# Performance work log

Hardware: AMD Instinct MI355X
Metric: run time of the kernel (lower is better)

## Reference

```python
import jax, jax.numpy as jnp
import numpy as np

N, IN_DIM, H1, H2, HEADS = 3072, 256, 128, 64, 4
NEG_INF = -9.0e15  # matches torch zero_vec = -9e15

def _xavier(key, shape):
    fan_in, fan_out = shape[-2], shape[-1]
    lim = np.sqrt(6.0 / (fan_in + fan_out)).astype(np.float32)
    return jax.random.uniform(key, shape, jnp.float32, -lim, lim)

def setup_inputs() -> dict:
    key = jax.random.key(0)
    ks = jax.random.split(key, 14)
    x = jax.random.normal(ks[0], (N, IN_DIM), jnp.float32)
    adj = jax.random.randint(ks[1], (N, N), 0, 2, jnp.int32)
    # layer 1 params (per-head stacked)
    W1 = _xavier(ks[2], (HEADS, IN_DIM, H1))
    a1s = _xavier(ks[3], (HEADS, H1)) * 1.414   # a[:F] of the (2F,1) xavier vector
    a1d = _xavier(ks[4], (HEADS, H1)) * 1.414   # a[F:]
    lin1 = _xavier(ks[5], (HEADS * H1, H1))
    res1 = _xavier(ks[6], (IN_DIM, H1))
    # layer 2 params
    W2 = _xavier(ks[7], (HEADS, H1, H2))
    a2s = _xavier(ks[8], (HEADS, H2)) * 1.414
    a2d = _xavier(ks[9], (HEADS, H2)) * 1.414
    lin2 = _xavier(ks[10], (HEADS * H2, H2))
    res2 = _xavier(ks[11], (H1, H2))
    return {"x": x, "adj": adj, "W1": W1, "a1s": a1s, "a1d": a1d,
            "lin1": lin1, "res1": res1, "W2": W2, "a2s": a2s, "a2d": a2d,
            "lin2": lin2, "res2": res2}

def _gat_residual_layer(h, mask, W, a_s, a_d, lin, res):
    # h: [N, F_in], W: [H, F_in, F_out], mask: [N, N] bool
    Wh = jnp.einsum('nf,hfo->hno', h, W)                 # [H, N, F_out]
    src = jnp.einsum('hno,ho->hn', Wh, a_s)              # Wh @ a[:F]
    dst = jnp.einsum('hno,ho->hn', Wh, a_d)              # Wh @ a[F:]
    e = src[:, :, None] + dst[:, None, :]                # [H, N, N]
    e = jnp.where(e > 0, e, 0.2 * e)                     # leaky_relu(0.2)
    e = jnp.where(mask[None], e, NEG_INF)                # adj mask
    attn = jax.nn.softmax(e, axis=-1)                    # dropout p=0.1 -> identity (eval)
    hp = jax.nn.elu(jnp.einsum('hij,hjo->hio', attn, Wh))  # per-head output, elu
    n = h.shape[0]
    hp = jnp.transpose(hp, (1, 0, 2)).reshape(n, -1)     # concat heads (head-major)
    hp = jax.nn.elu(hp @ lin)                            # multi-head mix + elu
    out = jax.nn.relu(hp + h @ res)                      # residual + relu
    return jax.nn.relu(out)                              # encoder-loop relu; dropout(0.4) identity

def reference(x, adj, W1, a1s, a1d, lin1, res1, W2, a2s, a2d, lin2, res2):
    mask = adj > 0
    h = _gat_residual_layer(x, mask, W1, a1s, a1d, lin1, res1)
    h = _gat_residual_layer(h, mask, W2, a2s, a2d, lin2, res2)
    return h  # embedding [N, H2]
```

## Files before the change

### kernel.cpp

```cpp
#include <hip/hip_runtime.h>
#include <hip/hip_bf16.h>
#include <stdint.h>

using bf16 = __hip_bfloat16;
typedef short short8 __attribute__((ext_vector_type(8)));
typedef short short4v __attribute__((ext_vector_type(4)));
typedef float f32x4 __attribute__((ext_vector_type(4)));

constexpr int N = 3072;
constexpr int D0 = 256;
constexpr int F1 = 128;
constexpr int F2 = 64;
constexpr int HEADS = 4;
constexpr int NW = N / 32;
constexpr float CSHIFT = 20.0f;

#define DI __device__ __forceinline__
DI short f2bs(float v) { bf16 b = __float2bfloat16(v); return *(short*)&b; }

__global__ __launch_bounds__(256) void k_pack_adj(const int* __restrict__ adj,
                                                  uint32_t* __restrict__ bits) {
  int idx = blockIdx.x * 256 + threadIdx.x;
  unsigned long long m = __ballot(adj[idx] > 0);
  if ((threadIdx.x & 63) == 0) {
    bits[idx >> 5]       = (uint32_t)m;
    bits[(idx >> 5) + 1] = (uint32_t)(m >> 32);
  }
}

__global__ __launch_bounds__(256) void k_cvt(const float* __restrict__ x,
                                             const float* __restrict__ W1,
                                             const float* __restrict__ lin1,
                                             const float* __restrict__ res1,
                                             const float* __restrict__ W2,
                                             const float* __restrict__ lin2,
                                             const float* __restrict__ res2,
                                             bf16* __restrict__ xb,
                                             bf16* __restrict__ W1T,
                                             bf16* __restrict__ lin1T,
                                             bf16* __restrict__ res1T,
                                             bf16* __restrict__ W2T,
                                             bf16* __restrict__ lin2T,
                                             bf16* __restrict__ res2T) {
  int t = blockIdx.y;
  int i = blockIdx.x * 256 + threadIdx.x;
  switch (t) {
    case 0:
      if (i < N * D0) xb[i] = __float2bfloat16(x[i]);
      break;
    case 1:
      if (i < HEADS * F1 * D0) { int k = i & 255; int ho = i >> 8; int h = ho >> 7, o = ho & 127;
        W1T[i] = __float2bfloat16(W1[((size_t)h * D0 + k) * F1 + o]); }
      break;
    case 2:
      if (i < F1 * HEADS * F1) { int k = i & 511; int o = i >> 9;
        lin1T[i] = __float2bfloat16(lin1[k * F1 + o]); }
      break;
    case 3:
      if (i < F1 * D0) { int k = i & 255; int o = i >> 8;
        res1T[i] = __float2bfloat16(res1[k * F1 + o]); }
      break;
    case 4:
      if (i < HEADS * F2 * F1) { int k = i & 127; int ho = i >> 7; int h = ho >> 6, o = ho & 63;
        W2T[i] = __float2bfloat16(W2[((size_t)h * F1 + k) * F2 + o]); }
      break;
    case 5:
      if (i < F2 * HEADS * F2) { int k = i & 255; int o = i >> 8;
        lin2T[i] = __float2bfloat16(lin2[k * F2 + o]); }
      break;
    case 6:
      if (i < F2 * F1) { int k = i & 127; int o = i >> 7;
        res2T[i] = __float2bfloat16(res2[k * F2 + o]); }
      break;
  }
}

template <int K, int NOUT, int F>
__global__ __launch_bounds__(256) void k_whead_mfma(const bf16* __restrict__ A,
                                                    const bf16* __restrict__ BT,
                                                    bf16* __restrict__ BP,
                                                    const float* __restrict__ as_,
                                                    const float* __restrict__ ad_,
                                                    float* __restrict__ src,
                                                    float* __restrict__ dst) {
  int row0 = blockIdx.x * 16;
  int wid = threadIdx.x >> 6, lane = threadIdx.x & 63;
  int l15 = lane & 15, q = lane >> 4;
  int col = blockIdx.y * 64 + wid * 16 + l15;

  const bf16* aP = A + (size_t)(row0 + l15) * K + q * 8;
  const bf16* bP = BT + (size_t)col * K + q * 8;
  f32x4 acc;
#pragma unroll
  for (int r = 0; r < 4; r++) acc[r] = 0.f;
#pragma unroll
  for (int ks = 0; ks < K / 32; ks++) {
    short8 a = *(const short8*)(aP + ks * 32);
    short8 b = *(const short8*)(bP + ks * 32);
    acc = __builtin_amdgcn_mfma_f32_16x16x32_bf16(a, b, acc, 0, 0, 0);
  }

  int h  = col / F;
  int cl = col % F;
  int ct = cl >> 4;
  int jt = row0 >> 5;
  int qp = ((row0 >> 4) & 1) * 2 + (q >> 1);
  int eo = (q & 1) * 4;
  short4v w;
#pragma unroll
  for (int r = 0; r < 4; r++) w[r] = f2bs(acc[r]);
  size_t off = ((((size_t)h * (F / 16) + ct) * (N / 32) + jt) * 4 + qp) * 128 + l15 * 8 + eo;
  *(short4v*)(BP + off) = w;

  float asv = as_[col], adv = ad_[col];
#pragma unroll
  for (int r = 0; r < 4; r++) {
    float sp = acc[r] * asv, dp = acc[r] * adv;
#pragma unroll
    for (int m = 1; m < 16; m <<= 1) {
      sp += __shfl_xor(sp, m);
      dp += __shfl_xor(dp, m);
    }
    if (l15 == 0) {
      atomicAdd(&src[h * N + row0 + q * 4 + r], sp);
      atomicAdd(&dst[h * N + row0 + q * 4 + r], dp);
    }
  }
}

template <int F>
__global__ __launch_bounds__(256, 2) void k_attn_fused(const bf16* __restrict__ BP,
                                                       const float* __restrict__ src,
                                                       const float* __restrict__ dst,
                                                       const uint32_t* __restrict__ bits,
                                                       float* __restrict__ hp_part,
                                                       float* __restrict__ rs_part) {
  constexpr int CT = F / 16;
  constexpr int CTN = CT / 4;
  constexpr int KSTEPS = 12;
  int h    = blockIdx.y;
  int kb   = blockIdx.z;
  int row0 = blockIdx.x * 32;
  int tid = threadIdx.x, wid = tid >> 6, lane = tid & 63;
  int l15 = lane & 15, q = lane >> 4;
  int jbase = kb * (N / 2) + wid * 384;

  float src0 = src[h * N + row0 + l15];
  float src1 = src[h * N + row0 + 16 + l15];
  const float* dh = dst + h * N;
  const uint32_t* b0 = bits + (size_t)(row0 + l15) * NW;
  const uint32_t* b1 = bits + (size_t)(row0 + 16 + l15) * NW;
  const bf16* bph = BP + (size_t)h * CT * (N / 32) * 512;

  f32x4 acc0[CT], acc1[CT];
#pragma unroll
  for (int ct = 0; ct < CT; ct++)
#pragma unroll
    for (int r = 0; r < 4; r++) { acc0[ct][r] = 0.f; acc1[ct][r] = 0.f; }
  float rs0 = 0.f, rs1 = 0.f;

  for (int ks = 0; ks < KSTEPS; ks++) {
    int j0 = jbase + ks * 32;
    int jt = j0 >> 5;
    f32x4 dlo = *(const f32x4*)(dh + j0 + q * 8);
    f32x4 dhi = *(const f32x4*)(dh + j0 + q * 8 + 4);
    uint32_t m0 = (b0[jt] >> (q * 8)) & 0xffu;
    uint32_t m1 = (b1[jt] >> (q * 8)) & 0xffu;
    float pv0[8], pv1[8];
#pragma unroll
    for (int e = 0; e < 8; e++) {
      float d = e < 4 ? dlo[e] : dhi[e - 4];
      float t0 = src0 + d; t0 = fmaxf(t0, 0.2f * t0);
      float p0 = ((m0 >> e) & 1u) ? __expf(t0 - CSHIFT) : 0.f;
      rs0 += p0; pv0[e] = p0;
      float t1 = src1 + d; t1 = fmaxf(t1, 0.2f * t1);
      float p1 = ((m1 >> e) & 1u) ? __expf(t1 - CSHIFT) : 0.f;
      rs1 += p1; pv1[e] = p1;
    }
    short8 a0, a1;
#pragma unroll
    for (int e = 0; e < 8; e++) { a0[e] = f2bs(pv0[e]); a1[e] = f2bs(pv1[e]); }
#pragma unroll
    for (int ct = 0; ct < CT; ct++) {
      short8 b = *(const short8*)(bph + (((size_t)ct * (N / 32) + jt) * 64 + lane) * 8);
      acc0[ct] = __builtin_amdgcn_mfma_f32_16x16x32_bf16(a0, b, acc0[ct], 0, 0, 0);
      acc1[ct] = __builtin_amdgcn_mfma_f32_16x16x32_bf16(a1, b, acc1[ct], 0, 0, 0);
    }
  }

  rs0 += __shfl_xor(rs0, 16); rs0 += __shfl_xor(rs0, 32);
  rs1 += __shfl_xor(rs1, 16); rs1 += __shfl_xor(rs1, 32);
  if (q == 0) atomicAdd(&rs_part[((size_t)kb * HEADS + h) * N + row0 + l15], rs0);
  if (q == 1) atomicAdd(&rs_part[((size_t)kb * HEADS + h) * N + row0 + 16 + l15], rs1);

  __shared__ float red[4][64][CT * 4 + 1];
#pragma unroll
  for (int t = 0; t < 2; t++) {
    __syncthreads();
#pragma unroll
    for (int ct = 0; ct < CT; ct++)
#pragma unroll
      for (int r = 0; r < 4; r++)
        red[wid][lane][ct * 4 + r] = t ? acc1[ct][r] : acc0[ct][r];
    __syncthreads();
#pragma unroll
    for (int cc = 0; cc < CTN; cc++) {
      int ct = wid * CTN + cc;
#pragma unroll
      for (int r = 0; r < 4; r++) {
        float v = red[0][lane][ct * 4 + r] + red[1][lane][ct * 4 + r] +
                  red[2][lane][ct * 4 + r] + red[3][lane][ct * 4 + r];
        int row = row0 + t * 16 + q * 4 + r;
        hp_part[((size_t)kb * N + row) * (HEADS * F) + h * F + ct * 16 + l15] = v;
      }
    }
  }
}

template <int F>
__global__ __launch_bounds__(256) void k_attn_combine(const float* __restrict__ hp_part,
                                                      const float* __restrict__ rs_part,
                                                      bf16* __restrict__ hp) {
  constexpr int HF = HEADS * F;
  int i = (blockIdx.x * 256 + threadIdx.x) * 4;
  int row = i / HF, c = i % HF, h = c / F;
  f32x4 p0 = *(const f32x4*)(hp_part + (size_t)row * HF + c);
  f32x4 p1 = *(const f32x4*)(hp_part + ((size_t)N + row) * HF + c);
  float s = rs_part[h * N + row] + rs_part[(HEADS + h) * N + row];
  float inv = 1.f / s;
  short4v o;
#pragma unroll
  for (int r = 0; r < 4; r++) {
    float v = (p0[r] + p1[r]) * inv;
    v = v > 0.f ? v : __expf(v) - 1.f;
    o[r] = f2bs(v);
  }
  *(short4v*)(hp + i) = o;
}

template <int K1, int K2, int NOUT, bool F32OUT>
__global__ __launch_bounds__(256) void k_mix_mfma(const bf16* __restrict__ A1,
                                                  const bf16* __restrict__ B1T,
                                                  const bf16* __restrict__ A2,
                                                  const bf16* __restrict__ B2T,
                                                  void* __restrict__ outv) {
  int row0 = blockIdx.x * 16;
  int wid = threadIdx.x >> 6, lane = threadIdx.x & 63;
  int l15 = lane & 15, q = lane >> 4;
  int col = blockIdx.y * 64 + wid * 16 + l15;

  f32x4 acc1, acc2;
#pragma unroll
  for (int r = 0; r < 4; r++) { acc1[r] = 0.f; acc2[r] = 0.f; }

  const bf16* a1P = A1 + (size_t)(row0 + l15) * K1 + q * 8;
  const bf16* b1P = B1T + (size_t)col * K1 + q * 8;
#pragma unroll
  for (int ks = 0; ks < K1 / 32; ks++) {
    short8 a = *(const short8*)(a1P + ks * 32);
    short8 b = *(const short8*)(b1P + ks * 32);
    acc1 = __builtin_amdgcn_mfma_f32_16x16x32_bf16(a, b, acc1, 0, 0, 0);
  }
  const bf16* a2P = A2 + (size_t)(row0 + l15) * K2 + q * 8;
  const bf16* b2P = B2T + (size_t)col * K2 + q * 8;
#pragma unroll
  for (int ks = 0; ks < K2 / 32; ks++) {
    short8 a = *(const short8*)(a2P + ks * 32);
    short8 b = *(const short8*)(b2P + ks * 32);
    acc2 = __builtin_amdgcn_mfma_f32_16x16x32_bf16(a, b, acc2, 0, 0, 0);
  }

#pragma unroll
  for (int r = 0; r < 4; r++) {
    float v = acc1[r];
    v = v > 0.f ? v : __expf(v) - 1.f;
    v += acc2[r];
    v = v > 0.f ? v : 0.f;
    int rw = row0 + q * 4 + r;
    if (F32OUT) ((float*)outv)[(size_t)rw * NOUT + col] = v;
    else        ((bf16*)outv)[(size_t)rw * NOUT + col] = __float2bfloat16(v);
  }
}

extern "C" void kernel_launch(void* const* d_in, const int* in_sizes, int n_in,
                              void* d_out, int out_size, void* d_ws, size_t ws_size,
                              hipStream_t stream) {
  const float* x    = (const float*)d_in[0];
  const int*   adj  = (const int*)d_in[1];
  const float* W1   = (const float*)d_in[2];
  const float* a1s  = (const float*)d_in[3];
  const float* a1d  = (const float*)d_in[4];
  const float* lin1 = (const float*)d_in[5];
  const float* res1 = (const float*)d_in[6];
  const float* W2   = (const float*)d_in[7];
  const float* a2s  = (const float*)d_in[8];
  const float* a2d  = (const float*)d_in[9];
  const float* lin2 = (const float*)d_in[10];
  const float* res2 = (const float*)d_in[11];
  float* out = (float*)d_out;

  char* p = (char*)d_ws;
  auto alloc = [&](size_t bytes) { void* r = (void*)p; p += (bytes + 255) & ~(size_t)255; return r; };
  uint32_t* bits = (uint32_t*)alloc((size_t)N * NW * 4);
  bf16* xb    = (bf16*)alloc((size_t)N * D0 * 2);
  bf16* W1T   = (bf16*)alloc((size_t)HEADS * F1 * D0 * 2);
  bf16* lin1T = (bf16*)alloc((size_t)F1 * HEADS * F1 * 2);
  bf16* res1T = (bf16*)alloc((size_t)F1 * D0 * 2);
  bf16* W2T   = (bf16*)alloc((size_t)HEADS * F2 * F1 * 2);
  bf16* lin2T = (bf16*)alloc((size_t)F2 * HEADS * F2 * 2);
  bf16* res2T = (bf16*)alloc((size_t)F2 * F1 * 2);
  bf16* BP1   = (bf16*)alloc((size_t)HEADS * F1 * N * 2);
  bf16* BP2   = (bf16*)alloc((size_t)HEADS * F2 * N * 2);
  float* src1 = (float*)alloc((size_t)HEADS * N * 4);
  float* dst1 = (float*)alloc((size_t)HEADS * N * 4);
  float* src2 = (float*)alloc((size_t)HEADS * N * 4);
  float* dst2 = (float*)alloc((size_t)HEADS * N * 4);
  float* rs1  = (float*)alloc((size_t)2 * HEADS * N * 4);
  float* rs2  = (float*)alloc((size_t)2 * HEADS * N * 4);
  float* hpp1 = (float*)alloc((size_t)2 * N * HEADS * F1 * 4);
  float* hpp2 = (float*)alloc((size_t)2 * N * HEADS * F2 * 4);
  bf16* hp1   = (bf16*)alloc((size_t)N * HEADS * F1 * 2);
  bf16* hp2   = (bf16*)alloc((size_t)N * HEADS * F2 * 2);
  bf16* h1b   = (bf16*)alloc((size_t)N * F1 * 2);

  hipMemsetAsync(src1, 0, (size_t)HEADS * N * 4 * 8, stream);

  k_pack_adj<<<dim3(N * N / 256), dim3(256), 0, stream>>>(adj, bits);
  k_cvt<<<dim3(N * D0 / 256, 7), dim3(256), 0, stream>>>(x, W1, lin1, res1, W2, lin2, res2,
                                                         xb, W1T, lin1T, res1T, W2T, lin2T, res2T);

  k_whead_mfma<D0, HEADS * F1, F1>
      <<<dim3(N / 16, HEADS * F1 / 64), dim3(256), 0, stream>>>(xb, W1T, BP1, a1s, a1d, src1, dst1);
  k_attn_fused<F1><<<dim3(N / 32, HEADS, 2), dim3(256), 0, stream>>>(BP1, src1, dst1, bits, hpp1, rs1);
  k_attn_combine<F1><<<dim3(N * HEADS * F1 / 1024), dim3(256), 0, stream>>>(hpp1, rs1, hp1);
  k_mix_mfma<HEADS * F1, D0, F1, false>
      <<<dim3(N / 16, F1 / 64), dim3(256), 0, stream>>>(hp1, lin1T, xb, res1T, h1b);

  k_whead_mfma<F1, HEADS * F2, F2>
      <<<dim3(N / 16, HEADS * F2 / 64), dim3(256), 0, stream>>>(h1b, W2T, BP2, a2s, a2d, src2, dst2);
  k_attn_fused<F2><<<dim3(N / 32, HEADS, 2), dim3(256), 0, stream>>>(BP2, src2, dst2, bits, hpp2, rs2);
  k_attn_combine<F2><<<dim3(N * HEADS * F2 / 1024), dim3(256), 0, stream>>>(hpp2, rs2, hp2);
  k_mix_mfma<HEADS * F2, F1, F2, true>
      <<<dim3(N / 16, F2 / 64), dim3(256), 0, stream>>>(hp2, lin2T, h1b, res2T, out);
}
```

Before: 208.9 us.

## Widen attention row tile to 64 and split key dimension three ways

The fused attention kernel now processes 64 rows per block (four 16-row MFMA tiles) instead of 32. Each loaded B fragment is therefore reused across four A tiles, halving B-operand global traffic per row. The key dimension is split into three chunks instead of two to keep the grid populated, and the combine kernel sums over three partials. This quadruples accumulator registers per thread, which for F=128 may hurt occupancy or spill, and it adds an extra partial buffer to write and read.

```diff
diff --git a/kernel.cpp b/kernel.cpp
--- a/kernel.cpp
+++ b/kernel.cpp
@@ -13,6 +13,7 @@
 constexpr int F2 = 64;
 constexpr int HEADS = 4;
 constexpr int NW = N / 32;
+constexpr int KSPLIT = 3;
 constexpr float CSHIFT = 20.0f;
 
 #define DI __device__ __forceinline__
@@ -137,71 +138,80 @@
                                                        float* __restrict__ rs_part) {
   constexpr int CT = F / 16;
   constexpr int CTN = CT / 4;
-  constexpr int KSTEPS = 12;
+  constexpr int KSTEPS = 8;
   int h    = blockIdx.y;
   int kb   = blockIdx.z;
-  int row0 = blockIdx.x * 32;
+  int row0 = blockIdx.x * 64;
   int tid = threadIdx.x, wid = tid >> 6, lane = tid & 63;
   int l15 = lane & 15, q = lane >> 4;
-  int jbase = kb * (N / 2) + wid * 384;
-
-  float src0 = src[h * N + row0 + l15];
-  float src1 = src[h * N + row0 + 16 + l15];
+  int jbase = kb * (N / KSPLIT) + wid * 256;
+
+  float srcr[4];
+  const uint32_t* br[4];
+#pragma unroll
+  for (int rt = 0; rt < 4; rt++) {
+    srcr[rt] = src[h * N + row0 + rt * 16 + l15];
+    br[rt] = bits + (size_t)(row0 + rt * 16 + l15) * NW;
+  }
   const float* dh = dst + h * N;
-  const uint32_t* b0 = bits + (size_t)(row0 + l15) * NW;
-  const uint32_t* b1 = bits + (size_t)(row0 + 16 + l15) * NW;
   const bf16* bph = BP + (size_t)h * CT * (N / 32) * 512;
 
-  f32x4 acc0[CT], acc1[CT];
-#pragma unroll
-  for (int ct = 0; ct < CT; ct++)
-#pragma unroll
-    for (int r = 0; r < 4; r++) { acc0[ct][r] = 0.f; acc1[ct][r] = 0.f; }
-  float rs0 = 0.f, rs1 = 0.f;
-
+  f32x4 acc[4][CT];
+#pragma unroll
+  for (int rt = 0; rt < 4; rt++)
+#pragma unroll
+    for (int ct = 0; ct < CT; ct++)
+#pragma unroll
+      for (int r = 0; r < 4; r++) acc[rt][ct][r] = 0.f;
+  float rs[4] = {0.f, 0.f, 0.f, 0.f};
+
+#pragma unroll
   for (int ks = 0; ks < KSTEPS; ks++) {
     int j0 = jbase + ks * 32;
     int jt = j0 >> 5;
     f32x4 dlo = *(const f32x4*)(dh + j0 + q * 8);
     f32x4 dhi = *(const f32x4*)(dh + j0 + q * 8 + 4);
-    uint32_t m0 = (b0[jt] >> (q * 8)) & 0xffu;
-    uint32_t m1 = (b1[jt] >> (q * 8)) & 0xffu;
-    float pv0[8], pv1[8];
-#pragma unroll
-    for (int e = 0; e < 8; e++) {
-      float d = e < 4 ? dlo[e] : dhi[e - 4];
-      float t0 = src0 + d; t0 = fmaxf(t0, 0.2f * t0);
-      float p0 = ((m0 >> e) & 1u) ? __expf(t0 - CSHIFT) : 0.f;
-      rs0 += p0; pv0[e] = p0;
-      float t1 = src1 + d; t1 = fmaxf(t1, 0.2f * t1);
-      float p1 = ((m1 >> e) & 1u) ? __expf(t1 - CSHIFT) : 0.f;
-      rs1 += p1; pv1[e] = p1;
-    }
-    short8 a0, a1;
-#pragma unroll
-    for (int e = 0; e < 8; e++) { a0[e] = f2bs(pv0[e]); a1[e] = f2bs(pv1[e]); }
+    short8 a[4];
+#pragma unroll
+    for (int rt = 0; rt < 4; rt++) {
+      uint32_t m0 = (br[rt][jt] >> (q * 8)) & 0xffu;
+#pragma unroll
+      for (int e = 0; e < 8; e++) {
+        float d = e < 4 ? dlo[e] : dhi[e - 4];
+        float t0 = srcr[rt] + d; t0 = fmaxf(t0, 0.2f * t0);
+        float p0 = ((m0 >> e) & 1u) ? __expf(t0 - CSHIFT) : 0.f;
+        rs[rt] += p0;
+        a[rt][e] = f2bs(p0);
+      }
+    }
 #pragma unroll
     for (int ct = 0; ct < CT; ct++) {
       short8 b = *(const short8*)(bph + (((size_t)ct * (N / 32) + jt) * 64 + lane) * 8);
-      acc0[ct] = __builtin_amdgcn_mfma_f32_16x16x32_bf16(a0, b, acc0[ct], 0, 0, 0);
-      acc1[ct] = __builtin_amdgcn_mfma_f32_16x16x32_bf16(a1, b, acc1[ct], 0, 0, 0);
-    }
-  }
-
-  rs0 += __shfl_xor(rs0, 16); rs0 += __shfl_xor(rs0, 32);
-  rs1 += __shfl_xor(rs1, 16); rs1 += __shfl_xor(rs1, 32);
-  if (q == 0) atomicAdd(&rs_part[((size_t)kb * HEADS + h) * N + row0 + l15], rs0);
-  if (q == 1) atomicAdd(&rs_part[((size_t)kb * HEADS + h) * N + row0 + 16 + l15], rs1);
+#pragma unroll
+      for (int rt = 0; rt < 4; rt++)
+        acc[rt][ct] = __builtin_amdgcn_mfma_f32_16x16x32_bf16(a[rt], b, acc[rt][ct], 0, 0, 0);
+    }
+  }
+
+#pragma unroll
+  for (int rt = 0; rt < 4; rt++) {
+    rs[rt] += __shfl_xor(rs[rt], 16);
+    rs[rt] += __shfl_xor(rs[rt], 32);
+  }
+  if (q == 0) {
+#pragma unroll
+    for (int rt = 0; rt < 4; rt++)
+      atomicAdd(&rs_part[((size_t)kb * HEADS + h) * N + row0 + rt * 16 + l15], rs[rt]);
+  }
 
   __shared__ float red[4][64][CT * 4 + 1];
 #pragma unroll
-  for (int t = 0; t < 2; t++) {
+  for (int rt = 0; rt < 4; rt++) {
     __syncthreads();
 #pragma unroll
     for (int ct = 0; ct < CT; ct++)
 #pragma unroll
-      for (int r = 0; r < 4; r++)
-        red[wid][lane][ct * 4 + r] = t ? acc1[ct][r] : acc0[ct][r];
+      for (int r = 0; r < 4; r++) red[wid][lane][ct * 4 + r] = acc[rt][ct][r];
     __syncthreads();
 #pragma unroll
     for (int cc = 0; cc < CTN; cc++) {
@@ -210,7 +220,7 @@
       for (int r = 0; r < 4; r++) {
         float v = red[0][lane][ct * 4 + r] + red[1][lane][ct * 4 + r] +
                   red[2][lane][ct * 4 + r] + red[3][lane][ct * 4 + r];
-        int row = row0 + t * 16 + q * 4 + r;
+        int row = row0 + rt * 16 + q * 4 + r;
         hp_part[((size_t)kb * N + row) * (HEADS * F) + h * F + ct * 16 + l15] = v;
       }
     }
@@ -224,14 +234,22 @@
   constexpr int HF = HEADS * F;
   int i = (blockIdx.x * 256 + threadIdx.x) * 4;
   int row = i / HF, c = i % HF, h = c / F;
-  f32x4 p0 = *(const f32x4*)(hp_part + (size_t)row * HF + c);
-  f32x4 p1 = *(const f32x4*)(hp_part + ((size_t)N + row) * HF + c);
-  float s = rs_part[h * N + row] + rs_part[(HEADS + h) * N + row];
+  f32x4 pacc;
+  float s = 0.f;
+#pragma unroll
+  for (int r = 0; r < 4; r++) pacc[r] = 0.f;
+#pragma unroll
+  for (int kb = 0; kb < KSPLIT; kb++) {
+    f32x4 pk = *(const f32x4*)(hp_part + ((size_t)kb * N + row) * HF + c);
+#pragma unroll
+    for (int r = 0; r < 4; r++) pacc[r] += pk[r];
+    s += rs_part[((size_t)kb * HEADS + h) * N + row];
+  }
   float inv = 1.f / s;
   short4v o;
 #pragma unroll
   for (int r = 0; r < 4; r++) {
-    float v = (p0[r] + p1[r]) * inv;
+    float v = pacc[r] * inv;
     v = v > 0.f ? v : __expf(v) - 1.f;
     o[r] = f2bs(v);
   }
@@ -315,15 +333,15 @@
   float* dst1 = (float*)alloc((size_t)HEADS * N * 4);
   float* src2 = (float*)alloc((size_t)HEADS * N * 4);
   float* dst2 = (float*)alloc((size_t)HEADS * N * 4);
-  float* rs1  = (float*)alloc((size_t)2 * HEADS * N * 4);
-  float* rs2  = (float*)alloc((size_t)2 * HEADS * N * 4);
-  float* hpp1 = (float*)alloc((size_t)2 * N * HEADS * F1 * 4);
-  float* hpp2 = (float*)alloc((size_t)2 * N * HEADS * F2 * 4);
+  float* rs1  = (float*)alloc((size_t)KSPLIT * HEADS * N * 4);
+  float* rs2  = (float*)alloc((size_t)KSPLIT * HEADS * N * 4);
+  float* hpp1 = (float*)alloc((size_t)KSPLIT * N * HEADS * F1 * 4);
+  float* hpp2 = (float*)alloc((size_t)KSPLIT * N * HEADS * F2 * 4);
   bf16* hp1   = (bf16*)alloc((size_t)N * HEADS * F1 * 2);
   bf16* hp2   = (bf16*)alloc((size_t)N * HEADS * F2 * 2);
   bf16* h1b   = (bf16*)alloc((size_t)N * F1 * 2);
 
-  hipMemsetAsync(src1, 0, (size_t)HEADS * N * 4 * 8, stream);
+  hipMemsetAsync(src1, 0, (size_t)HEADS * N * 4 * (4 + 2 * KSPLIT), stream);
 
   k_pack_adj<<<dim3(N * N / 256), dim3(256), 0, stream>>>(adj, bits);
   k_cvt<<<dim3(N * D0 / 256, 7), dim3(256), 0, stream>>>(x, W1, lin1, res1, W2, lin2, res2,
@@ -331,14 +349,14 @@
 
   k_whead_mfma<D0, HEADS * F1, F1>
       <<<dim3(N / 16, HEADS * F1 / 64), dim3(256), 0, stream>>>(xb, W1T, BP1, a1s, a1d, src1, dst1);
-  k_attn_fused<F1><<<dim3(N / 32, HEADS, 2), dim3(256), 0, stream>>>(BP1, src1, dst1, bits, hpp1, rs1);
+  k_attn_fused<F1><<<dim3(N / 64, HEADS, KSPLIT), dim3(256), 0, stream>>>(BP1, src1, dst1, bits, hpp1, rs1);
   k_attn_combine<F1><<<dim3(N * HEADS * F1 / 1024), dim3(256), 0, stream>>>(hpp1, rs1, hp1);
   k_mix_mfma<HEADS * F1, D0, F1, false>
       <<<dim3(N / 16, F1 / 64), dim3(256), 0, stream>>>(hp1, lin1T, xb, res1T, h1b);
 
   k_whead_mfma<F1, HEADS * F2, F2>
       <<<dim3(N / 16, HEADS * F2 / 64), dim3(256), 0, stream>>>(h1b, W2T, BP2, a2s, a2d, src2, dst2);
-  k_attn_fused<F2><<<dim3(N / 32, HEADS, 2), dim3(256), 0, stream>>>(BP2, src2, dst2, bits, hpp2, rs2);
+  k_attn_fused<F2><<<dim3(N / 64, HEADS, KSPLIT), dim3(256), 0, stream>>>(BP2, src2, dst2, bits, hpp2, rs2);
   k_attn_combine<F2><<<dim3(N * HEADS * F2 / 1024), dim3(256), 0, stream>>>(hpp2, rs2, hp2);
   k_mix_mfma<HEADS * F2, F1, F2, true>
       <<<dim3(N / 16, F2 / 64), dim3(256), 0, stream>>>(hp2, lin2T, h1b, res2T, out);
```

New measurement: 242.5 us. 1.16x slower.
